# Kernel optimization log

Hardware: AMD Instinct MI355X
Metric: run time of the kernel (lower is better)

Reference implementation:

```python
import jax, jax.numpy as jnp
import numpy as np

NUM_ROUNDS = 64
D_HIDDEN = 256
B = 16384

# MD5 message schedule g(i)
_SCHED = np.array([i if i < 16 else ((5*i+1) % 16 if i < 32 else ((3*i+5) % 16 if i < 48 else (7*i) % 16)) for i in range(64)], dtype=np.int32)
# MD5 per-round shift amounts
_SHIFT = np.array([7,12,17,22]*4 + [5,9,14,20]*4 + [4,11,16,23]*4 + [6,10,15,21]*4, dtype=np.float32)
# round_info[i] = [i/64, shift[i]/25], shape (64, 2)
_ROUND_INFO = np.stack([np.arange(64, dtype=np.float32) / 64.0, _SHIFT / 25.0], axis=-1)


def setup_inputs() -> dict:
    key = jax.random.key(0)
    ks = jax.random.split(key, 8)
    return {
        "message_bytes": jax.random.uniform(ks[0], (B, 64), dtype=jnp.float32),
        "initial_state": jax.random.uniform(ks[1], (B, 16), dtype=jnp.float32),
        "W1": jax.random.normal(ks[2], (NUM_ROUNDS, 22, D_HIDDEN), dtype=jnp.float32) * (1.0 / np.sqrt(22.0)),
        "b1": jax.random.normal(ks[3], (NUM_ROUNDS, D_HIDDEN), dtype=jnp.float32) * 0.02,
        "W2": jax.random.normal(ks[4], (NUM_ROUNDS, D_HIDDEN, D_HIDDEN), dtype=jnp.float32) * (1.0 / np.sqrt(float(D_HIDDEN))),
        "b2": jax.random.normal(ks[5], (NUM_ROUNDS, D_HIDDEN), dtype=jnp.float32) * 0.02,
        "W3": jax.random.normal(ks[6], (NUM_ROUNDS, D_HIDDEN, 16), dtype=jnp.float32) * (1.0 / np.sqrt(float(D_HIDDEN))),
        "b3": jax.random.normal(ks[7], (NUM_ROUNDS, 16), dtype=jnp.float32) * 0.02,
    }


def reference(message_bytes, initial_state, W1, b1, W2, b2, W3, b3):
    Bsz = message_bytes.shape[0]
    msg_words = message_bytes.reshape(Bsz, 16, 4)
    # pre-gather the scheduled word per round: (64, B, 4)
    words = jnp.transpose(msg_words[:, jnp.asarray(_SCHED), :], (1, 0, 2))
    round_info = jnp.asarray(_ROUND_INFO)  # (64, 2)

    def step(state, xs):
        word, rinfo, w1, c1, w2, c2, w3, c3 = xs
        x = jnp.concatenate([state, word, jnp.broadcast_to(rinfo, (state.shape[0], 2))], axis=-1)  # (B, 22)
        h = jax.nn.gelu(x @ w1 + c1, approximate=False)
        h = jax.nn.gelu(h @ w2 + c2, approximate=False)
        return h @ w3 + c3, None

    final_state, _ = jax.lax.scan(step, initial_state, (words, round_info, W1, b1, W2, b2, W3, b3))
    return final_state
```

## Files before the change

kernel.cpp:

```cpp
#include <hip/hip_runtime.h>
#include <stdint.h>


using bf16x8   = __attribute__((ext_vector_type(8))) __bf16;
using floatx4  = __attribute__((ext_vector_type(4))) float;
using ushort4v = __attribute__((ext_vector_type(4))) unsigned short;

__constant__ int c_sched[64] = {
  0,1,2,3,4,5,6,7,8,9,10,11,12,13,14,15,
  1,6,11,0,5,10,15,4,9,14,3,8,13,2,7,12,
  5,8,11,14,1,4,7,10,13,0,3,6,9,12,15,2,
  0,7,14,5,12,3,10,1,8,15,6,13,4,11,2,9
};
__constant__ float c_shift[64] = {
  7,12,17,22,7,12,17,22,7,12,17,22,7,12,17,22,
  5,9,14,20,5,9,14,20,5,9,14,20,5,9,14,20,
  4,11,16,23,4,11,16,23,4,11,16,23,4,11,16,23,
  6,10,15,21,6,10,15,21,6,10,15,21,6,10,15,21
};

__device__ __forceinline__ unsigned short bfbits(__bf16 b) {
  union { __bf16 b; unsigned short u; } v; v.b = b; return v.u;
}
__device__ __forceinline__ float gelu_f(float x) {
  float ax = fabsf(x);
  float t  = __builtin_amdgcn_rcpf(__builtin_fmaf(0.33270222f, ax, 1.0f));
  float e  = __builtin_amdgcn_exp2f(x * x * -0.72134752f);
  float poly = t * __builtin_fmaf(t, __builtin_fmaf(t, 0.7478556f, -0.0958798f),
                                  0.3480242f);
  float er = __builtin_fmaf(-poly, e, 1.0f);
  er = copysignf(er, x);
  float hx = 0.5f * x;
  return __builtin_fmaf(hx, er, hx);
}
__device__ __forceinline__ floatx4 mfma16(bf16x8 a, bf16x8 b, floatx4 c) {
  return __builtin_amdgcn_mfma_f32_16x16x32_bf16(a, b, c, 0, 0, 0);
}
struct BfPair { unsigned short h, l; };
__device__ __forceinline__ BfPair split2(float s) {
  __bf16 hb = (__bf16)s;
  __bf16 lb = (__bf16)(s - (float)hb);
  BfPair p; p.h = bfbits(hb); p.l = bfbits(lb); return p;
}

#define N1G (64*16*64)
#define N2G (64*16*8*64)
#define N3G (64*8*64)

__global__ void pack_w(const float* __restrict__ W1,
                       const float* __restrict__ W2,
                       const float* __restrict__ W3,
                       unsigned short* __restrict__ P) {
  int gid = blockIdx.x * blockDim.x + threadIdx.x;
  if (gid >= N1G + N2G + N3G) return;
  unsigned short v[8];
  unsigned short* dst;
  if (gid < N1G) {
    int lane = gid & 63, t = (gid >> 6) & 15, r = gid >> 10;
    int qq = lane >> 4, mm = lane & 15;
    #pragma unroll
    for (int j = 0; j < 8; ++j) {
      int k = 8*qq + j;
      v[j] = (k < 22) ? bfbits((__bf16)W1[(r*22 + k)*256 + 16*t + mm]) : (unsigned short)0;
    }
    dst = P + (size_t)gid * 8;
  } else if (gid < N1G + N2G) {
    int g = gid - N1G;
    int lane = g & 63, c = (g >> 6) & 7, t = (g >> 9) & 15, r = g >> 13;
    int qq = lane >> 4, mm = lane & 15;
    #pragma unroll
    for (int j = 0; j < 8; ++j) {
      int k = 32*c + 8*qq + j;
      v[j] = bfbits((__bf16)W2[((size_t)r*256 + k)*256 + 16*t + mm]);
    }
    dst = P + (size_t)(N1G + g) * 8;
  } else {
    int g = gid - N1G - N2G;
    int lane = g & 63, c = (g >> 6) & 7, r = g >> 9;
    int qq = lane >> 4, mm = lane & 15;
    #pragma unroll
    for (int j = 0; j < 8; ++j) {
      int k = 32*c + 8*qq + j;
      v[j] = bfbits((__bf16)W3[(r*256 + k)*16 + mm]);
    }
    dst = P + (size_t)(N1G + N2G + g) * 8;
  }
  ushort4v lo = { v[0],v[1],v[2],v[3] }, hi = { v[4],v[5],v[6],v[7] };
  *(ushort4v*)dst = lo;
  *(ushort4v*)(dst + 4) = hi;
}

#define NG  2
#define TT  2
#define SXW 36
#define SH 264
#define SM 66

__global__ __launch_bounds__(512, 4) void md5_main(
    const float* __restrict__ msg,
    const float* __restrict__ st0,
    const float* __restrict__ b1,
    const float* __restrict__ b2,
    const float* __restrict__ b3,
    const unsigned short* __restrict__ P,
    float* __restrict__ out)
{
  __shared__ unsigned short xh[NG][16][SXW], xl[NG][16][SXW];
  __shared__ unsigned short hA[NG][16][SH], hB[NG][16][SH];
  __shared__ unsigned short msgb[NG*16][SM], msgl[NG*16][SM];

  const int tid  = threadIdx.x;
  const int wv   = tid >> 6;
  const int lane = tid & 63;
  const int q    = lane >> 4;
  const int ln   = lane & 15;
  const int row0 = blockIdx.x * (NG*16);
  const int l3w  = (blockIdx.x & 1) << 1;
  const int scw  = l3w ^ 2;

  const unsigned short* P1 = P;
  const unsigned short* P2 = P + (size_t)N1G * 8;
  const unsigned short* P3 = P + (size_t)(N1G + N2G) * 8;

  for (int i = tid; i < NG*16*SXW; i += 512) {
    (&xh[0][0][0])[i] = 0; (&xl[0][0][0])[i] = 0;
  }
  {
    int idx = tid * 4, rr = idx >> 6, cc = idx & 63;
    floatx4 v0 = *(const floatx4*)(msg + (size_t)(row0 + rr)*64 + cc);
    #pragma unroll
    for (int j = 0; j < 4; ++j) {
      BfPair p0 = split2(v0[j]);
      msgb[rr][cc + j] = p0.h;  msgl[rr][cc + j] = p0.l;
    }
  }
  if (wv == 0) {
    #pragma unroll
    for (int g = 0; g < NG; ++g) {
      floatx4 v = *(const floatx4*)(st0 + (size_t)(row0 + g*16 + ln)*16 + 4*q);
      ushort4v h4, l4;
      #pragma unroll
      for (int e = 0; e < 4; ++e) { BfPair p = split2(v[e]); h4[e] = p.h; l4[e] = p.l; }
      *(ushort4v*)&xh[g][ln][4*q] = h4;
      *(ushort4v*)&xl[g][ln][4*q] = l4;
    }
  }
  __syncthreads();
  if (lane < NG*16) {
    int g = lane >> 4, n = lane & 15, rrow = lane;
    int s = c_sched[0];
    BfPair i1p = split2(c_shift[0] / 25.0f);
    #pragma unroll
    for (int j = 0; j < 4; ++j) {
      xh[g][n][16+j] = msgb[rrow][4*s+j];
      xl[g][n][16+j] = msgl[rrow][4*s+j];
    }
    xh[g][n][20] = 0;     xl[g][n][20] = 0;
    xh[g][n][21] = i1p.h; xl[g][n][21] = i1p.l;
  }

  bf16x8  a1c[TT];  floatx4 bb1c[TT], bb2c[TT];
  {
    const unsigned short* p1 = P1 + ((size_t)(TT*wv)*64 + lane)*8;
    #pragma unroll
    for (int tt = 0; tt < TT; ++tt) {
      a1c[tt]  = *(const bf16x8*)(p1 + (size_t)tt*512);
      bb1c[tt] = *(const floatx4*)(b1 + (TT*wv + tt)*16 + 4*q);
      bb2c[tt] = *(const floatx4*)(b2 + (TT*wv + tt)*16 + 4*q);
    }
  }

  #pragma unroll 1
  for (int r = 0; r < 64; ++r) {
    bf16x8 bxh[NG], bxl[NG];
    #pragma unroll
    for (int g = 0; g < NG; ++g) {
      bxh[g] = *(const bf16x8*)&xh[g][ln][8*q];
      bxl[g] = *(const bf16x8*)&xl[g][ln][8*q];
    }
    #pragma unroll
    for (int tt = 0; tt < TT; ++tt) {
      int f0 = (TT*wv + tt)*16 + 4*q;
      #pragma unroll
      for (int g = 0; g < NG; ++g) {
        floatx4 acc = bb1c[tt];
        acc = mfma16(a1c[tt], bxl[g], acc);
        acc = mfma16(a1c[tt], bxh[g], acc);
        ushort4v h4;
        #pragma unroll
        for (int e = 0; e < 4; ++e) h4[e] = bfbits((__bf16)gelu_f(acc[e]));
        *(ushort4v*)&hA[g][ln][f0] = h4;
      }
    }
    __syncthreads();

    bf16x8 Bf[NG][8];
    #pragma unroll
    for (int g = 0; g < NG; ++g)
      #pragma unroll
      for (int c = 0; c < 8; ++c) Bf[g][c] = *(const bf16x8*)&hA[g][ln][32*c + 8*q];

    const unsigned short* p2 = P2 + ((size_t)((r*16 + TT*wv)*8)*64 + lane)*8;
    #pragma unroll
    for (int tt = 0; tt < TT; ++tt) {
      bf16x8 a2[8];
      #pragma unroll
      for (int c = 0; c < 8; ++c)
        a2[c] = *(const bf16x8*)(p2 + (size_t)(tt*8 + c)*512);
      int f0 = (TT*wv + tt)*16 + 4*q;
      #pragma unroll
      for (int g = 0; g < NG; ++g) {
        floatx4 acc = bb2c[tt];
        #pragma unroll
        for (int c = 0; c < 8; ++c) acc = mfma16(a2[c], Bf[g][c], acc);
        ushort4v h4;
        #pragma unroll
        for (int e = 0; e < 4; ++e) h4[e] = bfbits((__bf16)gelu_f(acc[e]));
        *(ushort4v*)&hB[g][ln][f0] = h4;
      }
    }
    __syncthreads();

    if (r < 63) {
      const unsigned short* p1n = P1 + ((size_t)((r+1)*16 + TT*wv)*64 + lane)*8;
      #pragma unroll
      for (int tt = 0; tt < TT; ++tt) {
        a1c[tt]  = *(const bf16x8*)(p1n + (size_t)tt*512);
        bb1c[tt] = *(const floatx4*)(b1 + (r+1)*256 + (TT*wv + tt)*16 + 4*q);
        bb2c[tt] = *(const floatx4*)(b2 + (r+1)*256 + (TT*wv + tt)*16 + 4*q);
      }
    }

    if (wv == l3w || wv == l3w + 1) {
      const int g = wv - l3w;
      const unsigned short* p3 = P3 + ((size_t)(r*8)*64 + lane)*8;
      bf16x8 a3[8];
      #pragma unroll
      for (int c = 0; c < 8; ++c) a3[c] = *(const bf16x8*)(p3 + (size_t)c*512);
      floatx4 s = *(const floatx4*)(b3 + r*16 + 4*q);
      #pragma unroll
      for (int c = 0; c < 8; ++c) {
        bf16x8 bh = *(const bf16x8*)&hB[g][ln][32*c + 8*q];
        s = mfma16(a3[c], bh, s);
      }
      if (r == 63) {
        *(floatx4*)(out + (size_t)(row0 + g*16 + ln)*16 + 4*q) = s;
      } else {
        ushort4v h4, l4;
        #pragma unroll
        for (int e = 0; e < 4; ++e) { BfPair p = split2(s[e]); h4[e] = p.h; l4[e] = p.l; }
        *(ushort4v*)&xh[g][ln][4*q] = h4;
        *(ushort4v*)&xl[g][ln][4*q] = l4;
      }
    }
    if (wv == scw && lane < NG*16 && r < 63) {
      int g = lane >> 4, n = lane & 15, rrow = lane;
      int sc = c_sched[r+1];
      float i0 = (float)(r+1) * 0.015625f;
      BfPair i1p = split2(c_shift[r+1] / 25.0f);
      #pragma unroll
      for (int j = 0; j < 4; ++j) {
        xh[g][n][16+j] = msgb[rrow][4*sc+j];
        xl[g][n][16+j] = msgl[rrow][4*sc+j];
      }
      xh[g][n][20] = bfbits((__bf16)i0); xl[g][n][20] = 0;
      xh[g][n][21] = i1p.h;              xl[g][n][21] = i1p.l;
    }
    if (r < 63) __syncthreads();
  }
}

extern "C" void kernel_launch(void* const* d_in, const int* in_sizes, int n_in,
                              void* d_out, int out_size, void* d_ws, size_t ws_size,
                              hipStream_t stream) {
  const float* msg = (const float*)d_in[0];
  const float* st0 = (const float*)d_in[1];
  const float* W1  = (const float*)d_in[2];
  const float* b1  = (const float*)d_in[3];
  const float* W2  = (const float*)d_in[4];
  const float* b2  = (const float*)d_in[5];
  const float* W3  = (const float*)d_in[6];
  const float* b3  = (const float*)d_in[7];
  float* out = (float*)d_out;
  (void)in_sizes; (void)n_in; (void)out_size; (void)ws_size;

  unsigned short* P = (unsigned short*)d_ws;
  const int totalGroups = N1G + N2G + N3G;
  pack_w<<<(totalGroups + 255) / 256, 256, 0, stream>>>(W1, W2, W3, P);
  md5_main<<<512, 512, 0, stream>>>(msg, st0, b1, b2, b3, P, out);
}
```

Measured before the change: 418.8 us.

## Switch MLP chain to fp16 MFMA, drop hi/lo split, pack GELU in half2

After: 408.6 us. 1.02x faster.

```diff
diff --git a/kernel.cpp b/kernel.cpp
--- a/kernel.cpp
+++ b/kernel.cpp
@@ -2,9 +2,12 @@
 #include <stdint.h>
 
 
-using bf16x8   = __attribute__((ext_vector_type(8))) __bf16;
+using f16x8    = __attribute__((ext_vector_type(8))) _Float16;
+using f16x2    = __attribute__((ext_vector_type(2))) _Float16;
+using fp16x2r  = __attribute__((ext_vector_type(2))) __fp16;
 using floatx4  = __attribute__((ext_vector_type(4))) float;
 using ushort4v = __attribute__((ext_vector_type(4))) unsigned short;
+using uint2v   = __attribute__((ext_vector_type(2))) unsigned int;
 
 __constant__ int c_sched[64] = {
   0,1,2,3,4,5,6,7,8,9,10,11,12,13,14,15,
@@ -19,28 +22,37 @@
   6,10,15,21,6,10,15,21,6,10,15,21,6,10,15,21
 };
 
-__device__ __forceinline__ unsigned short bfbits(__bf16 b) {
-  union { __bf16 b; unsigned short u; } v; v.b = b; return v.u;
-}
-__device__ __forceinline__ float gelu_f(float x) {
-  float ax = fabsf(x);
-  float t  = __builtin_amdgcn_rcpf(__builtin_fmaf(0.33270222f, ax, 1.0f));
-  float e  = __builtin_amdgcn_exp2f(x * x * -0.72134752f);
-  float poly = t * __builtin_fmaf(t, __builtin_fmaf(t, 0.7478556f, -0.0958798f),
-                                  0.3480242f);
-  float er = __builtin_fmaf(-poly, e, 1.0f);
-  er = copysignf(er, x);
-  float hx = 0.5f * x;
-  return __builtin_fmaf(hx, er, hx);
-}
-__device__ __forceinline__ floatx4 mfma16(bf16x8 a, bf16x8 b, floatx4 c) {
-  return __builtin_amdgcn_mfma_f32_16x16x32_bf16(a, b, c, 0, 0, 0);
-}
-struct BfPair { unsigned short h, l; };
-__device__ __forceinline__ BfPair split2(float s) {
-  __bf16 hb = (__bf16)s;
-  __bf16 lb = (__bf16)(s - (float)hb);
-  BfPair p; p.h = bfbits(hb); p.l = bfbits(lb); return p;
+__device__ __forceinline__ unsigned short f16bits(float x) {
+  union { _Float16 h; unsigned short u; } v; v.h = (_Float16)x; return v.u;
+}
+__device__ __forceinline__ f16x2 pkrtz(float a, float b) {
+  union { fp16x2r r; f16x2 h; } v; v.r = __builtin_amdgcn_cvt_pkrtz(a, b);
+  return v.h;
+}
+#define H2(c) ((f16x2){(_Float16)(c), (_Float16)(c)})
+
+__device__ __forceinline__ unsigned int gelu2(float a0, float a1) {
+  float t0 = __builtin_amdgcn_rcpf(__builtin_fmaf(0.33270222f, fabsf(a0), 1.0f));
+  float t1 = __builtin_amdgcn_rcpf(__builtin_fmaf(0.33270222f, fabsf(a1), 1.0f));
+  float e0 = __builtin_amdgcn_exp2f(a0 * a0 * -0.72134752f);
+  float e1 = __builtin_amdgcn_exp2f(a1 * a1 * -0.72134752f);
+  f16x2 xp = pkrtz(a0, a1);
+  f16x2 tp = pkrtz(t0, t1);
+  f16x2 ep = pkrtz(e0, e1);
+  f16x2 poly = tp * __builtin_elementwise_fma(
+                   tp, __builtin_elementwise_fma(tp, H2(0.7478556f), H2(-0.0958798f)),
+                   H2(0.3480242f));
+  f16x2 er = __builtin_elementwise_fma(poly, -ep, H2(1.0f));
+  union { f16x2 h; unsigned int u; } ue, ux, uo;
+  ue.h = er; ux.h = xp;
+  uo.u = (ue.u & 0x7FFF7FFFu) | (ux.u & 0x80008000u);
+  f16x2 hx = xp * H2(0.5f);
+  union { f16x2 h; unsigned int u; } r;
+  r.h = __builtin_elementwise_fma(hx, uo.h, hx);
+  return r.u;
+}
+__device__ __forceinline__ floatx4 mfma16f(f16x8 a, f16x8 b, floatx4 c) {
+  return __builtin_amdgcn_mfma_f32_16x16x32_f16(a, b, c, 0, 0, 0);
 }
 
 #define N1G (64*16*64)
@@ -61,7 +73,7 @@
     #pragma unroll
     for (int j = 0; j < 8; ++j) {
       int k = 8*qq + j;
-      v[j] = (k < 22) ? bfbits((__bf16)W1[(r*22 + k)*256 + 16*t + mm]) : (unsigned short)0;
+      v[j] = (k < 22) ? f16bits(W1[(r*22 + k)*256 + 16*t + mm]) : (unsigned short)0;
     }
     dst = P + (size_t)gid * 8;
   } else if (gid < N1G + N2G) {
@@ -71,7 +83,7 @@
     #pragma unroll
     for (int j = 0; j < 8; ++j) {
       int k = 32*c + 8*qq + j;
-      v[j] = bfbits((__bf16)W2[((size_t)r*256 + k)*256 + 16*t + mm]);
+      v[j] = f16bits(W2[((size_t)r*256 + k)*256 + 16*t + mm]);
     }
     dst = P + (size_t)(N1G + g) * 8;
   } else {
@@ -81,7 +93,7 @@
     #pragma unroll
     for (int j = 0; j < 8; ++j) {
       int k = 32*c + 8*qq + j;
-      v[j] = bfbits((__bf16)W3[(r*256 + k)*16 + mm]);
+      v[j] = f16bits(W3[(r*256 + k)*16 + mm]);
     }
     dst = P + (size_t)(N1G + N2G + g) * 8;
   }
@@ -92,7 +104,7 @@
 
 #define NG  2
 #define TT  2
-#define SXW 36
+#define SXW 32
 #define SH 264
 #define SM 66
 
@@ -105,9 +117,9 @@
     const unsigned short* __restrict__ P,
     float* __restrict__ out)
 {
-  __shared__ unsigned short xh[NG][16][SXW], xl[NG][16][SXW];
+  __shared__ unsigned short xh[NG][16][SXW];
   __shared__ unsigned short hA[NG][16][SH], hB[NG][16][SH];
-  __shared__ unsigned short msgb[NG*16][SM], msgl[NG*16][SM];
+  __shared__ unsigned short msgb[NG*16][SM];
 
   const int tid  = threadIdx.x;
   const int wv   = tid >> 6;
@@ -122,49 +134,40 @@
   const unsigned short* P2 = P + (size_t)N1G * 8;
   const unsigned short* P3 = P + (size_t)(N1G + N2G) * 8;
 
-  for (int i = tid; i < NG*16*SXW; i += 512) {
-    (&xh[0][0][0])[i] = 0; (&xl[0][0][0])[i] = 0;
-  }
+  for (int i = tid; i < NG*16*SXW; i += 512) (&xh[0][0][0])[i] = 0;
   {
     int idx = tid * 4, rr = idx >> 6, cc = idx & 63;
     floatx4 v0 = *(const floatx4*)(msg + (size_t)(row0 + rr)*64 + cc);
     #pragma unroll
-    for (int j = 0; j < 4; ++j) {
-      BfPair p0 = split2(v0[j]);
-      msgb[rr][cc + j] = p0.h;  msgl[rr][cc + j] = p0.l;
-    }
+    for (int j = 0; j < 4; ++j) msgb[rr][cc + j] = f16bits(v0[j]);
   }
   if (wv == 0) {
     #pragma unroll
     for (int g = 0; g < NG; ++g) {
       floatx4 v = *(const floatx4*)(st0 + (size_t)(row0 + g*16 + ln)*16 + 4*q);
-      ushort4v h4, l4;
-      #pragma unroll
-      for (int e = 0; e < 4; ++e) { BfPair p = split2(v[e]); h4[e] = p.h; l4[e] = p.l; }
+      ushort4v h4;
+      #pragma unroll
+      for (int e = 0; e < 4; ++e) h4[e] = f16bits(v[e]);
       *(ushort4v*)&xh[g][ln][4*q] = h4;
-      *(ushort4v*)&xl[g][ln][4*q] = l4;
     }
   }
   __syncthreads();
   if (lane < NG*16) {
     int g = lane >> 4, n = lane & 15, rrow = lane;
     int s = c_sched[0];
-    BfPair i1p = split2(c_shift[0] / 25.0f);
-    #pragma unroll
-    for (int j = 0; j < 4; ++j) {
-      xh[g][n][16+j] = msgb[rrow][4*s+j];
-      xl[g][n][16+j] = msgl[rrow][4*s+j];
-    }
-    xh[g][n][20] = 0;     xl[g][n][20] = 0;
-    xh[g][n][21] = i1p.h; xl[g][n][21] = i1p.l;
-  }
-
-  bf16x8  a1c[TT];  floatx4 bb1c[TT], bb2c[TT];
+    unsigned short i1b = f16bits(c_shift[0] / 25.0f);
+    #pragma unroll
+    for (int j = 0; j < 4; ++j) xh[g][n][16+j] = msgb[rrow][4*s+j];
+    xh[g][n][20] = 0;
+    xh[g][n][21] = i1b;
+  }
+
+  f16x8   a1c[TT];  floatx4 bb1c[TT], bb2c[TT];
   {
     const unsigned short* p1 = P1 + ((size_t)(TT*wv)*64 + lane)*8;
     #pragma unroll
     for (int tt = 0; tt < TT; ++tt) {
-      a1c[tt]  = *(const bf16x8*)(p1 + (size_t)tt*512);
+      a1c[tt]  = *(const f16x8*)(p1 + (size_t)tt*512);
       bb1c[tt] = *(const floatx4*)(b1 + (TT*wv + tt)*16 + 4*q);
       bb2c[tt] = *(const floatx4*)(b2 + (TT*wv + tt)*16 + 4*q);
     }
@@ -172,51 +175,42 @@
 
   #pragma unroll 1
   for (int r = 0; r < 64; ++r) {
-    bf16x8 bxh[NG], bxl[NG];
-    #pragma unroll
-    for (int g = 0; g < NG; ++g) {
-      bxh[g] = *(const bf16x8*)&xh[g][ln][8*q];
-      bxl[g] = *(const bf16x8*)&xl[g][ln][8*q];
-    }
+    f16x8 bx[NG];
+    #pragma unroll
+    for (int g = 0; g < NG; ++g) bx[g] = *(const f16x8*)&xh[g][ln][8*q];
     #pragma unroll
     for (int tt = 0; tt < TT; ++tt) {
       int f0 = (TT*wv + tt)*16 + 4*q;
       #pragma unroll
       for (int g = 0; g < NG; ++g) {
-        floatx4 acc = bb1c[tt];
-        acc = mfma16(a1c[tt], bxl[g], acc);
-        acc = mfma16(a1c[tt], bxh[g], acc);
-        ushort4v h4;
-        #pragma unroll
-        for (int e = 0; e < 4; ++e) h4[e] = bfbits((__bf16)gelu_f(acc[e]));
-        *(ushort4v*)&hA[g][ln][f0] = h4;
+        floatx4 acc = mfma16f(a1c[tt], bx[g], bb1c[tt]);
+        uint2v w = { gelu2(acc[0], acc[1]), gelu2(acc[2], acc[3]) };
+        *(uint2v*)&hA[g][ln][f0] = w;
       }
     }
     __syncthreads();
 
-    bf16x8 Bf[NG][8];
+    f16x8 Bf[NG][8];
     #pragma unroll
     for (int g = 0; g < NG; ++g)
       #pragma unroll
-      for (int c = 0; c < 8; ++c) Bf[g][c] = *(const bf16x8*)&hA[g][ln][32*c + 8*q];
+      for (int c = 0; c < 8; ++c) Bf[g][c] = *(const f16x8*)&hA[g][ln][32*c + 8*q];
 
     const unsigned short* p2 = P2 + ((size_t)((r*16 + TT*wv)*8)*64 + lane)*8;
     #pragma unroll
     for (int tt = 0; tt < TT; ++tt) {
-      bf16x8 a2[8];
+      f16x8 a2[8];
       #pragma unroll
       for (int c = 0; c < 8; ++c)
-        a2[c] = *(const bf16x8*)(p2 + (size_t)(tt*8 + c)*512);
+        a2[c] = *(const f16x8*)(p2 + (size_t)(tt*8 + c)*512);
       int f0 = (TT*wv + tt)*16 + 4*q;
       #pragma unroll
       for (int g = 0; g < NG; ++g) {
         floatx4 acc = bb2c[tt];
         #pragma unroll
-        for (int c = 0; c < 8; ++c) acc = mfma16(a2[c], Bf[g][c], acc);
-        ushort4v h4;
-        #pragma unroll
-        for (int e = 0; e < 4; ++e) h4[e] = bfbits((__bf16)gelu_f(acc[e]));
-        *(ushort4v*)&hB[g][ln][f0] = h4;
+        for (int c = 0; c < 8; ++c) acc = mfma16f(a2[c], Bf[g][c], acc);
+        uint2v w = { gelu2(acc[0], acc[1]), gelu2(acc[2], acc[3]) };
+        *(uint2v*)&hB[g][ln][f0] = w;
       }
     }
     __syncthreads();
@@ -225,7 +219,7 @@
       const unsigned short* p1n = P1 + ((size_t)((r+1)*16 + TT*wv)*64 + lane)*8;
       #pragma unroll
       for (int tt = 0; tt < TT; ++tt) {
-        a1c[tt]  = *(const bf16x8*)(p1n + (size_t)tt*512);
+        a1c[tt]  = *(const f16x8*)(p1n + (size_t)tt*512);
         bb1c[tt] = *(const floatx4*)(b1 + (r+1)*256 + (TT*wv + tt)*16 + 4*q);
         bb2c[tt] = *(const floatx4*)(b2 + (r+1)*256 + (TT*wv + tt)*16 + 4*q);
       }
@@ -234,37 +228,33 @@
     if (wv == l3w || wv == l3w + 1) {
       const int g = wv - l3w;
       const unsigned short* p3 = P3 + ((size_t)(r*8)*64 + lane)*8;
-      bf16x8 a3[8];
-      #pragma unroll
-      for (int c = 0; c < 8; ++c) a3[c] = *(const bf16x8*)(p3 + (size_t)c*512);
+      f16x8 a3[8];
+      #pragma unroll
+      for (int c = 0; c < 8; ++c) a3[c] = *(const f16x8*)(p3 + (size_t)c*512);
       floatx4 s = *(const floatx4*)(b3 + r*16 + 4*q);
       #pragma unroll
       for (int c = 0; c < 8; ++c) {
-        bf16x8 bh = *(const bf16x8*)&hB[g][ln][32*c + 8*q];
-        s = mfma16(a3[c], bh, s);
+        f16x8 bh = *(const f16x8*)&hB[g][ln][32*c + 8*q];
+        s = mfma16f(a3[c], bh, s);
       }
       if (r == 63) {
         *(floatx4*)(out + (size_t)(row0 + g*16 + ln)*16 + 4*q) = s;
       } else {
-        ushort4v h4, l4;
+        ushort4v h4;
         #pragma unroll
-        for (int e = 0; e < 4; ++e) { BfPair p = split2(s[e]); h4[e] = p.h; l4[e] = p.l; }
+        for (int e = 0; e < 4; ++e) h4[e] = f16bits(s[e]);
         *(ushort4v*)&xh[g][ln][4*q] = h4;
-        *(ushort4v*)&xl[g][ln][4*q] = l4;
       }
     }
     if (wv == scw && lane < NG*16 && r < 63) {
       int g = lane >> 4, n = lane & 15, rrow = lane;
       int sc = c_sched[r+1];
       float i0 = (float)(r+1) * 0.015625f;
-      BfPair i1p = split2(c_shift[r+1] / 25.0f);
-      #pragma unroll
-      for (int j = 0; j < 4; ++j) {
-        xh[g][n][16+j] = msgb[rrow][4*sc+j];
-        xl[g][n][16+j] = msgl[rrow][4*sc+j];
-      }
-      xh[g][n][20] = bfbits((__bf16)i0); xl[g][n][20] = 0;
-      xh[g][n][21] = i1p.h;              xl[g][n][21] = i1p.l;
+      unsigned short i1b = f16bits(c_shift[r+1] / 25.0f);
+      #pragma unroll
+      for (int j = 0; j < 4; ++j) xh[g][n][16+j] = msgb[rrow][4*sc+j];
+      xh[g][n][20] = f16bits(i0);
+      xh[g][n][21] = i1b;
     }
     if (r < 63) __syncthreads();
   }
```
